# Optimization experiments

Hardware: AMD Instinct MI355X
Metric: run time of the kernel (lower is better)

Reference implementation:

```python
import jax, jax.numpy as jnp
import numpy as np

D_MODEL = 1024
N_HEAD = 16
DFF = 4096
N_EXPERTS = 4
DFF_E = DFF // N_EXPERTS  # 1024, per-expert hidden
LN_EPS = 1e-5


def _layer_norm(x, g, b):
    m = jnp.mean(x, axis=-1, keepdims=True)
    v = jnp.mean(jnp.square(x - m), axis=-1, keepdims=True)
    return (x - m) * jax.lax.rsqrt(v + LN_EPS) * g + b


def setup_inputs() -> dict:
    key = jax.random.key(0)
    ks = jax.random.split(key, 16)
    B, S, D = 8, 1024, D_MODEL
    s = 0.02
    return {
        "src": jax.random.normal(ks[0], (B, S, D), jnp.float32),
        "pos_embed": jax.random.normal(ks[1], (B, S, D), jnp.float32),
        # nn.MultiheadAttention packed in-projection [3D, D] and out-projection [D, D]
        "in_proj_w": jax.random.normal(ks[2], (3 * D, D), jnp.float32) * s,
        "in_proj_b": jax.random.normal(ks[3], (3 * D,), jnp.float32) * s,
        "out_proj_w": jax.random.normal(ks[4], (D, D), jnp.float32) * s,
        "out_proj_b": jax.random.normal(ks[5], (D,), jnp.float32) * s,
        # MoE gate Linear(D, E)
        "gate_w": jax.random.normal(ks[6], (N_EXPERTS, D), jnp.float32) * s,
        "gate_b": jax.random.normal(ks[7], (N_EXPERTS,), jnp.float32) * s,
        # per-expert FFN: Linear(D, DFF_E) then Linear(DFF_E, D), stacked over experts
        "w1": jax.random.normal(ks[8], (N_EXPERTS, DFF_E, D), jnp.float32) * s,
        "b1": jax.random.normal(ks[9], (N_EXPERTS, DFF_E), jnp.float32) * s,
        "w2": jax.random.normal(ks[10], (N_EXPERTS, D, DFF_E), jnp.float32) * s,
        "b2": jax.random.normal(ks[11], (N_EXPERTS, D), jnp.float32) * s,
        # LayerNorms
        "ln1_g": jnp.ones((D,), jnp.float32),
        "ln1_b": jnp.zeros((D,), jnp.float32),
        "ln2_g": jnp.ones((D,), jnp.float32),
        "ln2_b": jnp.zeros((D,), jnp.float32),
    }


def reference(src, pos_embed, in_proj_w, in_proj_b, out_proj_w, out_proj_b,
              gate_w, gate_b, w1, b1, w2, b2, ln1_g, ln1_b, ln2_g, ln2_b):
    B, S, D = src.shape
    H, hd = N_HEAD, D // N_HEAD
    residual = src
    # --- self-attention (post-norm path, dropout in eval mode => identity) ---
    qk = src + pos_embed  # q = k = src + pos_embed, value = src
    wq, wk, wv = jnp.split(in_proj_w, 3, axis=0)
    bq, bk, bv = jnp.split(in_proj_b, 3)
    q = (qk @ wq.T + bq).reshape(B, S, H, hd).transpose(0, 2, 1, 3)
    k = (qk @ wk.T + bk).reshape(B, S, H, hd).transpose(0, 2, 1, 3)
    v = (src @ wv.T + bv).reshape(B, S, H, hd).transpose(0, 2, 1, 3)
    scores = jnp.einsum('bhqd,bhkd->bhqk', q, k) / jnp.sqrt(jnp.asarray(hd, q.dtype))
    attn = jax.nn.softmax(scores, axis=-1)
    o = jnp.einsum('bhqk,bhkd->bhqd', attn, v).transpose(0, 2, 1, 3).reshape(B, S, D)
    o = o @ out_proj_w.T + out_proj_b
    x = _layer_norm(residual + o, ln1_g, ln1_b)
    # --- MoE FFN: sample one expert per token from gate softmax ---
    gate_logits = x @ gate_w.T + gate_b  # [B, S, E]
    chosen = jax.random.categorical(jax.random.key(42), gate_logits, axis=-1)  # [B, S] int
    oh = jax.nn.one_hot(chosen, N_EXPERTS, dtype=x.dtype)  # [B, S, E]
    # dense all-expert compute + one-hot select (equals gather/scatter math)
    h = jax.nn.relu(jnp.einsum('bsd,efd->bsef', x, w1) + b1)  # [B,S,E,DFF_E]
    y = jnp.einsum('bsef,edf->bsed', h, w2) + b2              # [B,S,E,D]
    moe_out = jnp.einsum('bsed,bse->bsd', y, oh)
    out = _layer_norm(x + moe_out, ln2_g, ln2_b)
    return out
```

## Files before the change

kernel.cpp:

```cpp
#include <hip/hip_runtime.h>
#include <cstdint>
#include <cstddef>


typedef _Float16 h16;
typedef h16 h16x8 __attribute__((ext_vector_type(8)));
typedef h16 h16x4 __attribute__((ext_vector_type(4)));
typedef __fp16 fp16x2 __attribute__((ext_vector_type(2)));
typedef float f32x4 __attribute__((ext_vector_type(4)));
typedef uint32_t u32;

#define DM 1024
#define NH 16
#define HD 64
#define SEQ 1024
#define BB 8
#define BS (BB*SEQ)
#define NBH (BB*NH)
#define NE 4
#define DFE 1024
#define QB 128
#define NCHUNK 16
#define SLDA 32
#define FLD 72
#define NPOS 9216

#define MFMA16(a,b,c) __builtin_amdgcn_mfma_f32_16x16x32_f16(a,b,c,0,0,0)

static constexpr size_t E = (size_t)BS*DM*2;
static constexpr size_t OFF_QKH = 0;
static constexpr size_t OFF_QKL = E;
static constexpr size_t OFF_SRCH= 2*E;
static constexpr size_t OFF_SRCL= 3*E;
static constexpr size_t OFF_W3H = 4*E;
static constexpr size_t OFF_W3L = 4*E + (size_t)3*DM*DM*2;
static constexpr size_t OFF_WOH = 4*E + (size_t)6*DM*DM*2;
static constexpr size_t OFF_WOL = 4*E + (size_t)7*DM*DM*2;
static constexpr size_t OFF_QH  = 5*E;
static constexpr size_t OFF_QL  = 6*E;
static constexpr size_t OFF_KH  = 7*E;
static constexpr size_t OFF_KL  = 8*E;
static constexpr size_t OFF_VH  = 9*E;
static constexpr size_t OFF_VL  = 10*E;
static constexpr size_t OFF_OH  = 0;
static constexpr size_t OFF_OL  = E;
static constexpr size_t OFF_ATT = 2*E;
static constexpr size_t OFF_X   = 5*E;
static constexpr size_t OFF_XH  = 7*E;
static constexpr size_t OFF_W1H = 8*E;
static constexpr size_t OFF_W2H = 8*E + (size_t)NE*DFE*DM*2;
static constexpr size_t OFF_HH  = 9*E;
static constexpr size_t OFF_Y   = 11*E;
static constexpr size_t OFF_CHOSEN = 13*E;
static constexpr size_t OFF_COUNTS = 13*E + 32768;
static constexpr size_t OFF_CURSOR = OFF_COUNTS + 16;
static constexpr size_t OFF_EOFF   = OFF_CURSOR + 16;
static constexpr size_t OFF_PLIST  = OFF_EOFF + 16;
static constexpr size_t WS_NEEDED  = OFF_PLIST + (size_t)NPOS*4;

__device__ __forceinline__ void store_split(h16* H, h16* L, size_t idx, float v) {
  h16 h = (h16)v;
  H[idx] = h;
  L[idx] = (h16)(v - (float)h);
}

__device__ __forceinline__ float wave_sum(float v) {
  #pragma unroll
  for (int o = 32; o; o >>= 1) v += __shfl_xor(v, o);
  return v;
}

__device__ __forceinline__ u32 pk2(float a, float b, float& fa, float& fb) {
  union { fp16x2 h; u32 w; } u;
  u.h = __builtin_amdgcn_cvt_pkrtz(a, b);
  fa = (float)u.h[0];
  fb = (float)u.h[1];
  return u.w;
}
__device__ __forceinline__ u32 pk2w(float a, float b) {
  union { fp16x2 h; u32 w; } u;
  u.h = __builtin_amdgcn_cvt_pkrtz(a, b);
  return u.w;
}

__device__ __forceinline__ void gload16(const void* g, void* l) {
  __builtin_amdgcn_global_load_lds(
      (const __attribute__((address_space(1))) u32*)g,
      (__attribute__((address_space(3))) u32*)l, 16, 0, 0);
}

__device__ __forceinline__ void gemm256_core(
    const h16* __restrict__ Ah, const h16* __restrict__ Al,
    const h16* __restrict__ Bh, const h16* __restrict__ Bl,
    int K, int lda, int ldb, int m0, int n0,
    f32x4 (&acc)[8][4], h16* lds)
{
  constexpr int BUF = 4*256*SLDA;
  const int tid = threadIdx.x, lane = tid & 63, wid = tid >> 6;
  const int wr = (wid >> 2) * 128, wc = (wid & 3) * 64;
  const int lr16 = lane >> 2, lgrp = lane & 3;
  const int plane = wid >> 1;
  const int half  = (wid & 1) * 128;
  const int sw = (lr16 >> 1) & 3;
  const h16* gp = (plane == 0) ? Ah : (plane == 1) ? Al : (plane == 2) ? Bh : Bl;
  const int ld  = (plane < 2) ? lda : ldb;
  const long g0 = (long)((plane < 2 ? m0 : n0) + half + lr16) * ld + ((lgrp ^ sw) << 3);
  const int lo = plane*(256*SLDA) + half*SLDA;
  const int fr = lane & 15, gi = lane >> 4;
  const int pcol = ((gi ^ ((lane >> 1) & 3)) << 3);
  const int nt = K >> 5;

  auto stage = [&](int t, int buf) {
    h16* lbase = lds + buf*BUF + lo;
    const long k0 = (long)t << 5;
    #pragma unroll
    for (int g = 0; g < 8; ++g)
      gload16(gp + g0 + (long)(g*16)*ld + k0, lbase + (g*16)*SLDA);
  };

  stage(0, 0);
  __syncthreads();
  int cur = 0;
  for (int t = 0; t < nt; ++t) {
    if (t + 1 < nt) stage(t + 1, cur ^ 1);
    h16* base = lds + cur*BUF;
    h16* sAh_ = base;
    h16* sAl_ = base + 256*SLDA;
    h16* sBh_ = base + 2*256*SLDA;
    h16* sBl_ = base + 3*256*SLDA;
    h16x8 bh[4], bl[4];
    #pragma unroll
    for (int j = 0; j < 4; ++j) {
      bh[j] = *(const h16x8*)(sBh_ + (wc + j*16 + fr)*SLDA + pcol);
      bl[j] = *(const h16x8*)(sBl_ + (wc + j*16 + fr)*SLDA + pcol);
    }
    __builtin_amdgcn_s_setprio(1);
    #pragma unroll
    for (int i = 0; i < 8; ++i) {
      h16x8 ah = *(const h16x8*)(sAh_ + (wr + i*16 + fr)*SLDA + pcol);
      h16x8 al = *(const h16x8*)(sAl_ + (wr + i*16 + fr)*SLDA + pcol);
      #pragma unroll
      for (int j = 0; j < 4; ++j) {
        acc[i][j] = MFMA16(ah, bh[j], acc[i][j]);
        acc[i][j] = MFMA16(ah, bl[j], acc[i][j]);
        acc[i][j] = MFMA16(al, bh[j], acc[i][j]);
      }
    }
    __builtin_amdgcn_s_setprio(0);
    __syncthreads();
    cur ^= 1;
  }
}

#define EPI_256 \
  const int lane = threadIdx.x & 63, wid = threadIdx.x >> 6; \
  const int wr = (wid>>2)*128, wc = (wid&3)*64; \
  const int fr = lane & 15, rb = (lane>>4)*4;

template<bool GATHER>
__device__ __forceinline__ void hgemm256_core(
    const h16* __restrict__ A, const h16* __restrict__ B,
    int K, int lda, int ldb, int m0, int n0, const int* __restrict__ rowmap,
    f32x4 (&acc)[8][4], h16* lds)
{
  constexpr int BUF = 2*256*SLDA;
  const int tid = threadIdx.x, lane = tid & 63, wid = tid >> 6;
  const int wr = (wid >> 2) * 128, wc = (wid & 3) * 64;
  const int lr16 = lane >> 2, lgrp = lane & 3;
  const int plane = wid >> 2;
  const int qrow  = (wid & 3) * 64;
  const int sw = (lr16 >> 1) & 3;
  const int colo = (lgrp ^ sw) << 3;
  const h16* gp = plane ? B : A;
  const int ld  = plane ? ldb : lda;
  long g0[4];
  #pragma unroll
  for (int g = 0; g < 4; ++g) {
    int lrow = qrow + g*16 + lr16;
    long grow;
    if (GATHER && plane == 0) {
      int t = rowmap[m0 + lrow]; if (t < 0) t = 0;
      grow = t;
    } else {
      grow = (plane ? n0 : m0) + lrow;
    }
    g0[g] = grow * (long)ld + colo;
  }
  const int lo = plane*(256*SLDA) + qrow*SLDA;
  const int fr = lane & 15, gi = lane >> 4;
  const int pcol = ((gi ^ ((lane >> 1) & 3)) << 3);
  const int nt = K >> 5;

  auto stage = [&](int t, int buf) {
    h16* lbase = lds + buf*BUF + lo;
    const long k0 = (long)t << 5;
    #pragma unroll
    for (int g = 0; g < 4; ++g)
      gload16(gp + g0[g] + k0, lbase + (g*16)*SLDA);
  };

  stage(0, 0);
  __syncthreads();
  int cur = 0;
  for (int t = 0; t < nt; ++t) {
    if (t + 1 < nt) stage(t + 1, cur ^ 1);
    h16* base = lds + cur*BUF;
    h16* sA_ = base;
    h16* sB_ = base + 256*SLDA;
    h16x8 b_[4];
    #pragma unroll
    for (int j = 0; j < 4; ++j)
      b_[j] = *(const h16x8*)(sB_ + (wc + j*16 + fr)*SLDA + pcol);
    __builtin_amdgcn_s_setprio(1);
    #pragma unroll
    for (int i = 0; i < 8; ++i) {
      h16x8 a_ = *(const h16x8*)(sA_ + (wr + i*16 + fr)*SLDA + pcol);
      #pragma unroll
      for (int j = 0; j < 4; ++j)
        acc[i][j] = MFMA16(a_, b_[j], acc[i][j]);
    }
    __builtin_amdgcn_s_setprio(0);
    __syncthreads();
    cur ^= 1;
  }
}

__global__ void k_zero8(int* __restrict__ p) {
  if (threadIdx.x < 8) p[threadIdx.x] = 0;
}

__global__ void k_split_in(const float* __restrict__ src, const float* __restrict__ pos,
                           h16* __restrict__ qkH, h16* __restrict__ qkL,
                           h16* __restrict__ sH,  h16* __restrict__ sL) {
  int i = blockIdx.x*256 + threadIdx.x;
  float4 s = ((const float4*)src)[i];
  float4 p = ((const float4*)pos)[i];
  float sv[4] = {s.x, s.y, s.z, s.w};
  float qv[4] = {s.x+p.x, s.y+p.y, s.z+p.z, s.w+p.w};
  h16x4 sh, sl, qh, ql;
  #pragma unroll
  for (int q = 0; q < 4; ++q) {
    float xs = sv[q] * 16.0f; h16 hs = (h16)xs;
    sh[q] = hs; sl[q] = (h16)(xs - (float)hs);
    float xq = qv[q] * 16.0f; h16 hq = (h16)xq;
    qh[q] = hq; ql[q] = (h16)(xq - (float)hq);
  }
  ((h16x4*)sH)[i] = sh; ((h16x4*)sL)[i] = sl;
  ((h16x4*)qkH)[i] = qh; ((h16x4*)qkL)[i] = ql;
}

__global__ void k_split2(const float* __restrict__ a,
                         h16* __restrict__ H, h16* __restrict__ L, float scale, int n4) {
  int i = blockIdx.x*256 + threadIdx.x;
  if (i >= n4) return;
  float4 v = ((const float4*)a)[i];
  float vv[4] = {v.x, v.y, v.z, v.w};
  h16x4 hv, lv;
  #pragma unroll
  for (int q = 0; q < 4; ++q) {
    float x = vv[q] * scale;
    h16 h = (h16)x;
    hv[q] = h;
    lv[q] = (h16)(x - (float)h);
  }
  ((h16x4*)H)[i] = hv;
  ((h16x4*)L)[i] = lv;
}

__global__ void k_tof16(const float* __restrict__ a, h16* __restrict__ H, float scale, int n4) {
  int i = blockIdx.x*256 + threadIdx.x;
  if (i >= n4) return;
  float4 v = ((const float4*)a)[i];
  h16x4 hv;
  hv[0] = (h16)(v.x*scale); hv[1] = (h16)(v.y*scale);
  hv[2] = (h16)(v.z*scale); hv[3] = (h16)(v.w*scale);
  ((h16x4*)H)[i] = hv;
}

__global__ __launch_bounds__(512, 2) void k_qkv(
    const h16* __restrict__ qkh, const h16* __restrict__ qkl,
    const h16* __restrict__ sh,  const h16* __restrict__ sl,
    const h16* __restrict__ Wh,  const h16* __restrict__ Wl, const float* __restrict__ bias,
    h16* __restrict__ Qh, h16* __restrict__ Ql, h16* __restrict__ Kh, h16* __restrict__ Kl,
    h16* __restrict__ Vh, h16* __restrict__ Vl)
{
  __shared__ h16 lds[2*4*256*SLDA];
  const int bid = blockIdx.x;
  const int xcd = bid & 7, loc = bid >> 3;
  const int m0 = (xcd*4 + (loc & 3)) * 256;
  const int n0 = (loc >> 2) * 256;
  const bool isV = (n0 >= 2048);
  f32x4 acc[8][4] = {};
  gemm256_core(isV ? sh : qkh, isV ? sl : qkl, Wh, Wl,
               1024, 1024, 1024, m0, n0, acc, lds);
  EPI_256;
  if (!isV) {
    const bool isK = (n0 >= 1024);
    h16* Hd = isK ? Kh : Qh;
    h16* Ld = isK ? Kl : Ql;
    #pragma unroll
    for (int i = 0; i < 8; ++i)
      #pragma unroll
      for (int j = 0; j < 4; ++j)
        #pragma unroll
        for (int r = 0; r < 4; ++r) {
          int row = m0 + wr + i*16 + rb + r;
          int col = n0 + wc + j*16 + fr;
          float c = acc[i][j][r] * (1.0f/1024.0f) + bias[col];
          int b = row >> 10, s = row & 1023;
          int cc = col & 1023, h = cc >> 6, d = cc & 63;
          long bh = (long)b*NH + h;
          store_split(Hd, Ld, (bh*SEQ + s)*HD + d, c * 16.0f);
        }
  } else {
    #pragma unroll
    for (int i = 0; i < 8; ++i)
      #pragma unroll
      for (int j = 0; j < 4; ++j) {
        int row0 = m0 + wr + i*16 + rb;
        int col  = n0 + wc + j*16 + fr;
        int cc = col & 1023, h = cc >> 6, d = cc & 63;
        float bcol = bias[col];
        h16x4 hv, lv;
        #pragma unroll
        for (int r = 0; r < 4; ++r) {
          float cs = (acc[i][j][r] * (1.0f/1024.0f) + bcol) * 16.0f;
          h16 hh = (h16)cs;
          hv[r] = hh;
          lv[r] = (h16)(cs - (float)hh);
        }
        int b = row0 >> 10, s0 = row0 & 1023;
        long base = ((long)(b*NH + h)*HD + d)*SEQ + s0;
        *(h16x4*)(Vh + base) = hv;
        *(h16x4*)(Vl + base) = lv;
      }
  }
}

__global__ __launch_bounds__(512) void k_attn(
    const h16* __restrict__ Qh, const h16* __restrict__ Ql,
    const h16* __restrict__ Kh, const h16* __restrict__ Kl,
    const h16* __restrict__ Vh, const h16* __restrict__ Vl,
    h16* __restrict__ Oh, h16* __restrict__ Ol)
{
  __shared__ h16 lds[4*64*FLD];
  h16* sKh = lds;            h16* sKl = lds + 64*FLD;
  h16* sVh = lds + 2*64*FLD; h16* sVl = lds + 3*64*FLD;
  const int bid = blockIdx.x;
  const int swz = (bid & 7) * 128 + (bid >> 3);
  const int bh = swz >> 3;
  const int q0 = (swz & 7) * QB;
  const int tid = threadIdx.x, lane = tid & 63, w = tid >> 6;
  const int fr = lane & 15, hg = lane >> 4;
  const int kg = hg << 3;
  const long qbase = ((long)bh*SEQ + q0 + w*16 + fr) * HD;
  h16x8 qh[2], ql[2];
  qh[0] = *(const h16x8*)(Qh + qbase + kg);
  qh[1] = *(const h16x8*)(Qh + qbase + 32 + kg);
  ql[0] = *(const h16x8*)(Ql + qbase + kg);
  ql[1] = *(const h16x8*)(Ql + qbase + 32 + kg);
  f32x4 o1[4] = {}, o2[4] = {};
  float mrow = -3.0e38f, lrow = 0.f;
  const int srow = tid >> 3, skc = (tid & 7) << 3;
  const long kbase = ((long)bh*SEQ + srow) * HD + skc;
  const long vbase = ((long)bh*HD + srow) * SEQ + skc;
  const int srcA = fr + ((hg & 1) << 5);
  const int srcB = srcA + 16;
  for (int kt = 0; kt < NCHUNK; ++kt) {
    const int n0 = kt * 64;
    __syncthreads();
    {
      const long ka = kbase + (long)n0*HD;
      *(uint4*)(sKh + srow*FLD + skc) = *(const uint4*)(Kh + ka);
      *(uint4*)(sKl + srow*FLD + skc) = *(const uint4*)(Kl + ka);
      const long va = vbase + n0;
      *(uint4*)(sVh + srow*FLD + skc) = *(const uint4*)(Vh + va);
      *(uint4*)(sVl + srow*FLD + skc) = *(const uint4*)(Vl + va);
    }
    __syncthreads();
    f32x4 s1[4] = {}, s2[4] = {};
    __builtin_amdgcn_s_setprio(1);
    #pragma unroll
    for (int ks = 0; ks < 2; ++ks)
      #pragma unroll
      for (int j = 0; j < 4; ++j) {
        h16x8 kh = *(const h16x8*)(sKh + (j*16 + fr)*FLD + ks*32 + kg);
        h16x8 kl = *(const h16x8*)(sKl + (j*16 + fr)*FLD + ks*32 + kg);
        s1[j] = MFMA16(kh, qh[ks], s1[j]);
        s2[j] = MFMA16(kh, ql[ks], s2[j]);
        s2[j] = MFMA16(kl, qh[ks], s2[j]);
      }
    __builtin_amdgcn_s_setprio(0);
    float p[4][4];
    float tmax = -3.0e38f;
    #pragma unroll
    for (int j = 0; j < 4; ++j)
      #pragma unroll
      for (int r = 0; r < 4; ++r) {
        float sc = (s1[j][r] + s2[j][r]) * (0.125f/256.0f);
        p[j][r] = sc;
        tmax = fmaxf(tmax, sc);
      }
    tmax = fmaxf(tmax, __shfl_xor(tmax, 16));
    tmax = fmaxf(tmax, __shfl_xor(tmax, 32));
    float mn = fmaxf(mrow, tmax);
    float sclf = __expf(mrow - mn);
    mrow = mn;
    float psum = 0.f;
    #pragma unroll
    for (int j = 0; j < 4; ++j)
      #pragma unroll
      for (int r = 0; r < 4; ++r) { float e = __expf(p[j][r] - mn); p[j][r] = e; psum += e; }
    psum += __shfl_xor(psum, 16);
    psum += __shfl_xor(psum, 32);
    lrow = lrow*sclf + psum;
    #pragma unroll
    for (int r = 0; r < 4; ++r) {
      float sq = __shfl(sclf, hg*4 + r);
      #pragma unroll
      for (int jd = 0; jd < 4; ++jd) { o1[jd][r] *= sq; o2[jd][r] *= sq; }
    }
    u32 hp[4][2], lp[4][2];
    #pragma unroll
    for (int j = 0; j < 4; ++j)
      #pragma unroll
      for (int rp = 0; rp < 2; ++rp) {
        float a = p[j][2*rp]   * 512.0f;
        float b = p[j][2*rp+1] * 512.0f;
        float fa, fb;
        hp[j][rp] = pk2(a, b, fa, fb);
        lp[j][rp] = pk2w(a - fa, b - fb);
      }
    #pragma unroll
    for (int ks = 0; ks < 2; ++ks) {
      const int j0 = 2*ks, j1 = 2*ks + 1;
      u32 hA0 = (u32)__shfl((int)hp[j0][0], srcA), hA1 = (u32)__shfl((int)hp[j0][1], srcA);
      u32 hB0 = (u32)__shfl((int)hp[j0][0], srcB), hB1 = (u32)__shfl((int)hp[j0][1], srcB);
      u32 hC0 = (u32)__shfl((int)hp[j1][0], srcA), hC1 = (u32)__shfl((int)hp[j1][1], srcA);
      u32 hD0 = (u32)__shfl((int)hp[j1][0], srcB), hD1 = (u32)__shfl((int)hp[j1][1], srcB);
      u32 lA0 = (u32)__shfl((int)lp[j0][0], srcA), lA1 = (u32)__shfl((int)lp[j0][1], srcA);
      u32 lB0 = (u32)__shfl((int)lp[j0][0], srcB), lB1 = (u32)__shfl((int)lp[j0][1], srcB);
      u32 lC0 = (u32)__shfl((int)lp[j1][0], srcA), lC1 = (u32)__shfl((int)lp[j1][1], srcA);
      u32 lD0 = (u32)__shfl((int)lp[j1][0], srcB), lD1 = (u32)__shfl((int)lp[j1][1], srcB);
      const bool hij = (hg & 2) != 0;
      union { u32 w[4]; h16x8 v; } pa, pb;
      pa.w[0] = hij ? hC0 : hA0;  pa.w[1] = hij ? hC1 : hA1;
      pa.w[2] = hij ? hD0 : hB0;  pa.w[3] = hij ? hD1 : hB1;
      pb.w[0] = hij ? lC0 : lA0;  pb.w[1] = hij ? lC1 : lA1;
      pb.w[2] = hij ? lD0 : lB0;  pb.w[3] = hij ? lD1 : lB1;
      __builtin_amdgcn_s_setprio(1);
      #pragma unroll
      for (int jd = 0; jd < 4; ++jd) {
        h16x8 vh = *(const h16x8*)(sVh + (jd*16 + fr)*FLD + ks*32 + kg);
        h16x8 vl = *(const h16x8*)(sVl + (jd*16 + fr)*FLD + ks*32 + kg);
        o1[jd] = MFMA16(pa.v, vh, o1[jd]);
        o2[jd] = MFMA16(pa.v, vl, o2[jd]);
        o2[jd] = MFMA16(pb.v, vh, o2[jd]);
      }
      __builtin_amdgcn_s_setprio(0);
    }
  }
  float lq[4];
  #pragma unroll
  for (int r = 0; r < 4; ++r) lq[r] = __shfl(lrow, hg*4 + r);
  const int b = bh >> 4, h = bh & 15;
  #pragma unroll
  for (int jd = 0; jd < 4; ++jd)
    #pragma unroll
    for (int r = 0; r < 4; ++r) {
      int qrow = q0 + w*16 + hg*4 + r;
      int d = jd*16 + fr;
      float ov = (o1[jd][r] + o2[jd][r]) / (512.0f*16.0f*lq[r]);
      store_split(Oh, Ol, ((long)b*SEQ + qrow)*DM + h*HD + d, ov*16.0f);
    }
}

__global__ __launch_bounds__(512, 2) void k_out(
    const h16* __restrict__ Oh, const h16* __restrict__ Ol,
    const h16* __restrict__ Wh, const h16* __restrict__ Wl,
    const float* __restrict__ bias, float* __restrict__ attn)
{
  __shared__ h16 lds[2*4*256*SLDA];
  const int bid = blockIdx.x;
  const int xcd = bid & 7, loc = bid >> 3;
  const int m0 = (xcd*4 + (loc & 3)) * 256;
  const int n0 = (loc >> 2) * 256;
  f32x4 acc[8][4] = {};
  gemm256_core(Oh, Ol, Wh, Wl, 1024, 1024, 1024, m0, n0, acc, lds);
  EPI_256;
  #pragma unroll
  for (int i = 0; i < 8; ++i)
    #pragma unroll
    for (int j = 0; j < 4; ++j)
      #pragma unroll
      for (int r = 0; r < 4; ++r) {
        int row = m0 + wr + i*16 + rb + r;
        int col = n0 + wc + j*16 + fr;
        attn[(long)row*DM + col] = acc[i][j][r] * (1.0f/1024.0f) + bias[col];
      }
}

__device__ __forceinline__ void threefry(u32 x0, u32 x1, u32& y0, u32& y1) {
  const u32 ks0 = 0u, ks1 = 42u, ks2 = 0x1BD11BDAu ^ 42u;
  x0 += ks0; x1 += ks1;
  #define TF_R(r) { x0 += x1; x1 = (x1 << r) | (x1 >> (32 - r)); x1 ^= x0; }
  TF_R(13) TF_R(15) TF_R(26) TF_R(6)  x0 += ks1; x1 += ks2 + 1u;
  TF_R(17) TF_R(29) TF_R(16) TF_R(24) x0 += ks2; x1 += ks0 + 2u;
  TF_R(13) TF_R(15) TF_R(26) TF_R(6)  x0 += ks0; x1 += ks1 + 3u;
  TF_R(17) TF_R(29) TF_R(16) TF_R(24) x0 += ks1; x1 += ks2 + 4u;
  TF_R(13) TF_R(15) TF_R(26) TF_R(6)  x0 += ks2; x1 += ks0 + 5u;
  #undef TF_R
  y0 = x0; y1 = x1;
}

__device__ __forceinline__ float gumbel_from(u32 bits) {
  float f = __uint_as_float((bits >> 9) | 0x3F800000u) - 1.0f;
  float u = (f > 0.0f) ? f : 1.17549435e-38f;
  float nl = (float)(-log((double)u));
  return -(float)log((double)nl);
}

__global__ __launch_bounds__(256) void k_ln1g(
    const float* __restrict__ A, const float* __restrict__ Badd,
    const float* __restrict__ g, const float* __restrict__ be,
    const float* __restrict__ gw, const float* __restrict__ gb,
    float* __restrict__ xout, h16* __restrict__ xh,
    int* __restrict__ chosen, int* __restrict__ counts)
{
  int wave = threadIdx.x >> 6, lane = threadIdx.x & 63;
  long row = (long)blockIdx.x*4 + wave;
  const float* ar = A + row*DM; const float* br = Badd + row*DM;
  float v[16]; float s = 0.0f;
  #pragma unroll
  for (int p = 0; p < 4; ++p) {
    int d = p*256 + lane*4;
    float4 a = *(const float4*)(ar + d);
    float4 b = *(const float4*)(br + d);
    float t0=a.x+b.x, t1=a.y+b.y, t2=a.z+b.z, t3=a.w+b.w;
    v[4*p+0]=t0; v[4*p+1]=t1; v[4*p+2]=t2; v[4*p+3]=t3;
    s += t0+t1+t2+t3;
  }
  s = wave_sum(s);
  float m = s * (1.0f/1024.0f);
  float q = 0.0f;
  #pragma unroll
  for (int i = 0; i < 16; ++i) { float dd = v[i]-m; q += dd*dd; }
  q = wave_sum(q);
  float rs = (float)(1.0 / sqrt((double)(q * (1.0f/1024.0f) + 1e-5f)));
  float pe[4] = {0.f, 0.f, 0.f, 0.f};
  #pragma unroll
  for (int p = 0; p < 4; ++p) {
    int d = p*256 + lane*4;
    float4 gv = *(const float4*)(g + d);
    float4 bv = *(const float4*)(be + d);
    float y0 = (v[4*p+0]-m)*rs*gv.x + bv.x;
    float y1 = (v[4*p+1]-m)*rs*gv.y + bv.y;
    float y2 = (v[4*p+2]-m)*rs*gv.z + bv.z;
    float y3 = (v[4*p+3]-m)*rs*gv.w + bv.w;
    float4 o = {y0,y1,y2,y3};
    *(float4*)(xout + row*DM + d) = o;
    h16x4 hv; hv[0]=(h16)(y0*16.f); hv[1]=(h16)(y1*16.f);
    hv[2]=(h16)(y2*16.f); hv[3]=(h16)(y3*16.f);
    *(h16x4*)(xh + row*DM + d) = hv;
    #pragma unroll
    for (int e = 0; e < 4; ++e) {
      float4 w4 = *(const float4*)(gw + e*DM + d);
      pe[e] += y0*w4.x + y1*w4.y + y2*w4.z + y3*w4.w;
    }
  }
  #pragma unroll
  for (int e = 0; e < 4; ++e) pe[e] = wave_sum(pe[e]);
  if (lane == 0) {
    float best = -3.0e38f; int arg = 0;
    #pragma unroll
    for (int e = 0; e < 4; ++e) {
      float logit = pe[e] + gb[e];
      u32 j = (u32)(4*row + e);
      u32 y0, y1;
      threefry(0u, j, y0, y1);
      float vv = gumbel_from(y0 ^ y1) + logit;
      if (vv > best) { best = vv; arg = e; }
    }
    chosen[(int)row] = arg;
    atomicAdd(&counts[arg], 1);
  }
}

__global__ __launch_bounds__(256) void k_ln(
    const float* __restrict__ A, const float* __restrict__ Badd,
    const float* __restrict__ g, const float* __restrict__ be,
    float* __restrict__ dout)
{
  int wave = threadIdx.x >> 6, lane = threadIdx.x & 63;
  long row = (long)blockIdx.x*4 + wave;
  const float* ar = A + row*DM; const float* br = Badd + row*DM;
  float v[16]; float s = 0.0f;
  #pragma unroll
  for (int p = 0; p < 4; ++p) {
    int d = p*256 + lane*4;
    float4 a = *(const float4*)(ar + d);
    float4 b = *(const float4*)(br + d);
    float t0=a.x+b.x, t1=a.y+b.y, t2=a.z+b.z, t3=a.w+b.w;
    v[4*p+0]=t0; v[4*p+1]=t1; v[4*p+2]=t2; v[4*p+3]=t3;
    s += t0+t1+t2+t3;
  }
  s = wave_sum(s);
  float m = s * (1.0f/1024.0f);
  float q = 0.0f;
  #pragma unroll
  for (int i = 0; i < 16; ++i) { float dd = v[i]-m; q += dd*dd; }
  q = wave_sum(q);
  float rs = (float)(1.0 / sqrt((double)(q * (1.0f/1024.0f) + 1e-5f)));
  #pragma unroll
  for (int p = 0; p < 4; ++p) {
    int d = p*256 + lane*4;
    float4 gv = *(const float4*)(g + d);
    float4 bv = *(const float4*)(be + d);
    float y0 = (v[4*p+0]-m)*rs*gv.x + bv.x;
    float y1 = (v[4*p+1]-m)*rs*gv.y + bv.y;
    float y2 = (v[4*p+2]-m)*rs*gv.z + bv.z;
    float y3 = (v[4*p+3]-m)*rs*gv.w + bv.w;
    float4 o = {y0,y1,y2,y3};
    *(float4*)(dout + row*DM + d) = o;
  }
}

__global__ void k_offsets(const int* __restrict__ counts, int* __restrict__ eoff) {
  if (threadIdx.x == 0 && blockIdx.x == 0) {
    int o = 0;
    for (int e = 0; e < 4; ++e) { eoff[e] = o; o += (counts[e] + 255) & ~255; }
  }
}

__global__ void k_fill(int* __restrict__ p, int n) {
  int i = blockIdx.x*256 + threadIdx.x;
  if (i < n) p[i] = -1;
}

__global__ void k_scatter(const int* __restrict__ chosen, const int* __restrict__ eoff,
                          int* __restrict__ cursor, int* __restrict__ plist) {
  int t = blockIdx.x*256 + threadIdx.x;
  if (t >= BS) return;
  int e = chosen[t];
  int slot = atomicAdd(&cursor[e], 1);
  plist[eoff[e] + slot] = t;
}

__global__ __launch_bounds__(512, 2) void k_e1(
    const h16* __restrict__ Xh, const h16* __restrict__ W1, const float* __restrict__ b1,
    const int* __restrict__ plist, const int* __restrict__ eoff, h16* __restrict__ Hh)
{
  __shared__ h16 lds[2*2*256*SLDA];
  const int n0 = blockIdx.x*256, m0 = blockIdx.y*256;
  const int e = (m0 >= eoff[1]) + (m0 >= eoff[2]) + (m0 >= eoff[3]);
  f32x4 acc[8][4] = {};
  hgemm256_core<true>(Xh, W1 + (long)e*DFE*DM, 1024, 1024, 1024, m0, n0, plist, acc, lds);
  EPI_256;
  #pragma unroll
  for (int i = 0; i < 8; ++i)
    #pragma unroll
    for (int j = 0; j < 4; ++j)
      #pragma unroll
      for (int r = 0; r < 4; ++r) {
        int row = m0 + wr + i*16 + rb + r;
        int col = n0 + wc + j*16 + fr;
        float c = acc[i][j][r] * (1.0f/1024.0f) + b1[e*DFE + col];
        c = fmaxf(c, 0.0f);
        Hh[(long)row*DFE + col] = (h16)(c * 16.0f);
      }
}

__global__ __launch_bounds__(512, 2) void k_e2(
    const h16* __restrict__ Hh, const h16* __restrict__ W2, const float* __restrict__ b2,
    const int* __restrict__ plist, const int* __restrict__ eoff, float* __restrict__ y)
{
  __shared__ h16 lds[2*2*256*SLDA];
  const int n0 = blockIdx.x*256, m0 = blockIdx.y*256;
  const int e = (m0 >= eoff[1]) + (m0 >= eoff[2]) + (m0 >= eoff[3]);
  f32x4 acc[8][4] = {};
  hgemm256_core<false>(Hh, W2 + (long)e*DM*DFE, 1024, DFE, DFE, m0, n0, nullptr, acc, lds);
  EPI_256;
  #pragma unroll
  for (int i = 0; i < 8; ++i)
    #pragma unroll
    for (int j = 0; j < 4; ++j)
      #pragma unroll
      for (int r = 0; r < 4; ++r) {
        int row = m0 + wr + i*16 + rb + r;
        int col = n0 + wc + j*16 + fr;
        int t = plist[row];
        if (t >= 0)
          y[(long)t*DM + col] = acc[i][j][r] * (1.0f/1024.0f) + b2[e*DM + col];
      }
}

extern "C" void kernel_launch(void* const* d_in, const int* in_sizes, int n_in,
                              void* d_out, int out_size, void* d_ws, size_t ws_size,
                              hipStream_t stream) {
  const float* src = (const float*)d_in[0];
  const float* pos = (const float*)d_in[1];
  const float* w3  = (const float*)d_in[2];
  const float* b3  = (const float*)d_in[3];
  const float* wo  = (const float*)d_in[4];
  const float* bo  = (const float*)d_in[5];
  const float* gw  = (const float*)d_in[6];
  const float* gb  = (const float*)d_in[7];
  const float* w1  = (const float*)d_in[8];
  const float* b1  = (const float*)d_in[9];
  const float* w2  = (const float*)d_in[10];
  const float* b2  = (const float*)d_in[11];
  const float* g1  = (const float*)d_in[12];
  const float* be1 = (const float*)d_in[13];
  const float* g2  = (const float*)d_in[14];
  const float* be2 = (const float*)d_in[15];
  float* out = (float*)d_out;
  char* ws = (char*)d_ws;
  if (ws_size < WS_NEEDED) return;

  auto H = [&](size_t off) { return (h16*)(ws + off); };
  auto F = [&](size_t off) { return (float*)(ws + off); };
  auto I = [&](size_t off) { return (int*)(ws + off); };

  k_zero8<<<1, 64, 0, stream>>>(I(OFF_COUNTS));

  k_split_in<<<BS*DM/4/256, 256, 0, stream>>>(src, pos,
      H(OFF_QKH), H(OFF_QKL), H(OFF_SRCH), H(OFF_SRCL));
  k_split2<<<3*DM*DM/4/256, 256, 0, stream>>>(w3, H(OFF_W3H), H(OFF_W3L), 64.0f, 3*DM*DM/4);
  k_split2<<<DM*DM/4/256, 256, 0, stream>>>(wo, H(OFF_WOH), H(OFF_WOL), 64.0f, DM*DM/4);

  k_qkv<<<dim3(384), 512, 0, stream>>>(
      H(OFF_QKH), H(OFF_QKL), H(OFF_SRCH), H(OFF_SRCL), H(OFF_W3H), H(OFF_W3L), b3,
      H(OFF_QH), H(OFF_QL), H(OFF_KH), H(OFF_KL), H(OFF_VH), H(OFF_VL));

  k_attn<<<dim3(NBH*(SEQ/QB)), 512, 0, stream>>>(
      H(OFF_QH), H(OFF_QL), H(OFF_KH), H(OFF_KL), H(OFF_VH), H(OFF_VL),
      H(OFF_OH), H(OFF_OL));

  k_out<<<dim3(128), 512, 0, stream>>>(
      H(OFF_OH), H(OFF_OL), H(OFF_WOH), H(OFF_WOL), bo, F(OFF_ATT));
  k_ln1g<<<BS/4, 256, 0, stream>>>(src, F(OFF_ATT), g1, be1, gw, gb,
      F(OFF_X), H(OFF_XH), I(OFF_CHOSEN), I(OFF_COUNTS));

  k_offsets<<<1, 64, 0, stream>>>(I(OFF_COUNTS), I(OFF_EOFF));
  k_fill<<<(NPOS+255)/256, 256, 0, stream>>>(I(OFF_PLIST), NPOS);
  k_scatter<<<BS/256, 256, 0, stream>>>(I(OFF_CHOSEN), I(OFF_EOFF), I(OFF_CURSOR), I(OFF_PLIST));

  k_tof16<<<NE*DFE*DM/4/256, 256, 0, stream>>>(w1, H(OFF_W1H), 64.0f, NE*DFE*DM/4);
  k_tof16<<<NE*DM*DFE/4/256, 256, 0, stream>>>(w2, H(OFF_W2H), 64.0f, NE*DM*DFE/4);
  k_e1<<<dim3(DFE/256, NPOS/256), 512, 0, stream>>>(
      H(OFF_XH), H(OFF_W1H), b1, I(OFF_PLIST), I(OFF_EOFF), H(OFF_HH));
  k_e2<<<dim3(DM/256, NPOS/256), 512, 0, stream>>>(
      H(OFF_HH), H(OFF_W2H), b2, I(OFF_PLIST), I(OFF_EOFF), F(OFF_Y));

  k_ln<<<BS/4, 256, 0, stream>>>(F(OFF_X), F(OFF_Y), g2, be2, out);
}
```

Baseline: 693.5 us.

## Prefetch next K/V tile into registers and defer softmax rescaling

Global loads of the next K/V tile are issued into registers right after the shared-memory store barrier, so they overlap with the current tile's MFMA and softmax work. Separately, the running-max update and accumulator rescale are skipped when the new tile max exceeds the stored max by at most 4 for every lane in the wave, which avoids the shuffles and multiplies of rescaling. This adds register pressure for the prefetched data and allows larger unnormalized exponentials to be packed into fp16 for the PV product.

```diff
diff --git a/kernel.cpp b/kernel.cpp
--- a/kernel.cpp
+++ b/kernel.cpp
@@ -366,18 +366,24 @@
   const long vbase = ((long)bh*HD + srow) * SEQ + skc;
   const int srcA = fr + ((hg & 1) << 5);
   const int srcB = srcA + 16;
+  uint4 rKh, rKl, rVh, rVl;
+  auto loadt = [&](int kt) {
+    const long ka = kbase + (long)(kt*64)*HD;
+    rKh = *(const uint4*)(Kh + ka);
+    rKl = *(const uint4*)(Kl + ka);
+    const long va = vbase + kt*64;
+    rVh = *(const uint4*)(Vh + va);
+    rVl = *(const uint4*)(Vl + va);
+  };
+  loadt(0);
   for (int kt = 0; kt < NCHUNK; ++kt) {
-    const int n0 = kt * 64;
     __syncthreads();
-    {
-      const long ka = kbase + (long)n0*HD;
-      *(uint4*)(sKh + srow*FLD + skc) = *(const uint4*)(Kh + ka);
-      *(uint4*)(sKl + srow*FLD + skc) = *(const uint4*)(Kl + ka);
-      const long va = vbase + n0;
-      *(uint4*)(sVh + srow*FLD + skc) = *(const uint4*)(Vh + va);
-      *(uint4*)(sVl + srow*FLD + skc) = *(const uint4*)(Vl + va);
-    }
+    *(uint4*)(sKh + srow*FLD + skc) = rKh;
+    *(uint4*)(sKl + srow*FLD + skc) = rKl;
+    *(uint4*)(sVh + srow*FLD + skc) = rVh;
+    *(uint4*)(sVl + srow*FLD + skc) = rVl;
     __syncthreads();
+    if (kt + 1 < NCHUNK) loadt(kt + 1);
     f32x4 s1[4] = {}, s2[4] = {};
     __builtin_amdgcn_s_setprio(1);
     #pragma unroll
@@ -403,9 +409,17 @@
       }
     tmax = fmaxf(tmax, __shfl_xor(tmax, 16));
     tmax = fmaxf(tmax, __shfl_xor(tmax, 32));
-    float mn = fmaxf(mrow, tmax);
-    float sclf = __expf(mrow - mn);
-    mrow = mn;
+    float mn;
+    const bool defer = (__all(tmax - mrow <= 4.0f) != 0);
+    float sclf;
+    if (defer) {
+      mn = mrow;
+      sclf = 1.0f;
+    } else {
+      mn = fmaxf(mrow, tmax);
+      sclf = __expf(mrow - mn);
+      mrow = mn;
+    }
     float psum = 0.f;
     #pragma unroll
     for (int j = 0; j < 4; ++j)
@@ -414,11 +428,13 @@
     psum += __shfl_xor(psum, 16);
     psum += __shfl_xor(psum, 32);
     lrow = lrow*sclf + psum;
-    #pragma unroll
-    for (int r = 0; r < 4; ++r) {
-      float sq = __shfl(sclf, hg*4 + r);
-      #pragma unroll
-      for (int jd = 0; jd < 4; ++jd) { o1[jd][r] *= sq; o2[jd][r] *= sq; }
+    if (!defer) {
+      #pragma unroll
+      for (int r = 0; r < 4; ++r) {
+        float sq = __shfl(sclf, hg*4 + r);
+        #pragma unroll
+        for (int jd = 0; jd < 4; ++jd) { o1[jd][r] *= sq; o2[jd][r] *= sq; }
+      }
     }
     u32 hp[4][2], lp[4][2];
     #pragma unroll
```

Result: no change. 690.6 us (-0.4%).
